# Kernel optimization log

Measured on AMD Instinct MI355X. Metric: run time of the kernel, lower is better.

The kernel has to match this reference:

```python
import jax, jax.numpy as jnp
import numpy as np

B, S, D = 4, 2048, 2048
E = 64           # num_experts
TOPK = 2         # num_experts_per_token


def setup_inputs() -> dict:
    key = jax.random.key(0)
    k1, k2, k3 = jax.random.split(key, 3)
    x_real = jax.random.normal(k1, (B, S, D), dtype=jnp.float32)
    x_imag = jax.random.normal(k2, (B, S, D), dtype=jnp.float32)
    # flax Dense: kernel [in_features, out_features] with lecun_normal-ish scale
    W = jax.random.normal(k3, (2 * D, E), dtype=jnp.float32) / np.sqrt(2.0 * D)
    b = jnp.zeros((E,), dtype=jnp.float32)
    return {"x_real": x_real, "x_imag": x_imag, "W": W, "b": b}


def reference(x_real, x_imag, W, b):
    # amp = |x|, phase = angle(x) for x = x_real + i*x_imag
    amp = jnp.hypot(x_real, x_imag)                 # [B,S,D]
    phase = jnp.arctan2(x_imag, x_real)             # [B,S,D]
    routing_input = jnp.concatenate([amp, phase], axis=-1)  # [B,S,2D]
    scores = jnp.einsum('bsf,fe->bse', routing_input, W) + b  # [B,S,E]
    probs = jax.nn.softmax(scores, axis=-1)
    top_k_probs, top_k_indices = jax.lax.top_k(probs, TOPK)   # [B,S,K]
    top_k_probs = top_k_probs / jnp.sum(top_k_probs, axis=-1, keepdims=True)
    return (top_k_probs, top_k_indices)
```

## Files before the change

kernel.cpp:

```cpp
#include <hip/hip_runtime.h>
#include <math.h>

#define NTOK 8192
#define DD   2048
#define EE   64
#define TSTRIP 16
#define NCH 16
#define PROB_N (NTOK*2)
#define AROW 136
#define F_PSTRIDE (128*4*64*8)

typedef _Float16 f16x8 __attribute__((ext_vector_type(8)));
typedef _Float16 f16x4 __attribute__((ext_vector_type(4)));
typedef float    f32x4 __attribute__((ext_vector_type(4)));

__device__ __forceinline__ float fast_atan2f(float y, float x) {
    const float ax = __builtin_fabsf(x), ay = __builtin_fabsf(y);
    const float hi = fmaxf(ax, ay), lo = fminf(ax, ay);
    const bool  big = lo > 0.4142135679721832f * hi;
    const float num = big ? (lo - hi) : lo;
    const float den = big ? (lo + hi) : hi;
    float rc = __builtin_amdgcn_rcpf(den);
    rc = rc * fmaf(-den, rc, 2.0f);
    const float z  = num * rc;
    const float z2 = z * z;
    float p = fmaf(z2, 8.05374449538e-2f, -1.38776856032e-1f);
    p = fmaf(z2, p, 1.99777106478e-1f);
    p = fmaf(z2, p, -3.33329491539e-1f);
    float r = fmaf(z * z2, p, z);
    r = r + (big ? 0.78539816339744830962f : 0.0f);
    r = (ay > ax) ? (1.57079632679489661923f - r) : r;
    r = (x < 0.0f) ? (3.14159265358979323846f - r) : r;
    return copysignf(r, y);
}

__device__ __forceinline__ void fsplit2(float x, _Float16& h1, _Float16& h2s) {
    const _Float16 a = (_Float16)x;
    h1 = a;
    h2s = (_Float16)((x - (float)a) * 2048.0f);
}

__global__ __launch_bounds__(256) void wsplit(const float* __restrict__ W,
                                              _Float16* __restrict__ F) {
    const int g  = blockIdx.x * 256 + threadIdx.x;
    const int e  = g & 63;
    const int q  = g >> 6;
    const int d0 = q * 4;
    const int nt = e >> 4;
    const int lane = ((d0 & 31) >> 3) * 16 + (e & 15);
    const int j0 = d0 & 7;
    const int cka = 2 * (d0 >> 5);

    f16x4 a1, a2, p1, p2;
    #pragma unroll
    for (int i = 0; i < 4; ++i) {
        _Float16 h, l;
        fsplit2(W[(size_t)(d0 + i) * EE + e], h, l);      a1[i] = h; a2[i] = l;
        fsplit2(W[(size_t)(DD + d0 + i) * EE + e], h, l); p1[i] = h; p2[i] = l;
    }
    *(f16x4*)&F[((size_t)(0 * 128 + cka)     * 4 + nt) * 512 + lane * 8 + j0] = a1;
    *(f16x4*)&F[((size_t)(1 * 128 + cka)     * 4 + nt) * 512 + lane * 8 + j0] = a2;
    *(f16x4*)&F[((size_t)(0 * 128 + cka + 1) * 4 + nt) * 512 + lane * 8 + j0] = p1;
    *(f16x4*)&F[((size_t)(1 * 128 + cka + 1) * 4 + nt) * 512 + lane * 8 + j0] = p2;
}

__global__ __launch_bounds__(512, 4) void gemm_topk(
    const float* __restrict__ xr, const float* __restrict__ xi,
    const _Float16* __restrict__ F, const float* __restrict__ bias,
    float* __restrict__ out)
{
    __shared__ __align__(16) _Float16 A[2][2][2][TSTRIP][AROW];
    __shared__ float scoreH[2][TSTRIP][EE];

    const int tid = threadIdx.x;
    const int t0  = blockIdx.x * TSTRIP;
    const int wv = tid >> 6, lane = tid & 63;
    const int nt = wv & 3, kh = wv >> 2;
    const int fm = lane & 15, fq = lane >> 4;
    const int kh_s  = tid >> 8;
    const int tok_s = (tid >> 4) & 15;
    const int f4    = tid & 15;

    const float bv = bias[lane];

    const float* prx = xr + (size_t)(t0 + tok_s) * DD + kh_s * 1024 + f4 * 4;
    const float* pix = xi + (size_t)(t0 + tok_s) * DD + kh_s * 1024 + f4 * 4;
    const int posa = 64 * (f4 >> 3) + (f4 & 7) * 4;

    auto sprocess = [&](float4 vr, float4 vi, int buf) {
        const float ar[4] = {vr.x, vr.y, vr.z, vr.w};
        const float ai[4] = {vi.x, vi.y, vi.z, vi.w};
        f16x4 a1, a2, p1, p2;
        #pragma unroll
        for (int i = 0; i < 4; ++i) {
            const float amp = __builtin_amdgcn_sqrtf(fmaf(ar[i], ar[i], ai[i] * ai[i]));
            const float ph  = fast_atan2f(ai[i], ar[i]);
            _Float16 h, l;
            fsplit2(amp, h, l); a1[i] = h; a2[i] = l;
            fsplit2(ph,  h, l); p1[i] = h; p2[i] = l;
        }
        *(f16x4*)&A[buf][kh_s][0][tok_s][posa]      = a1;
        *(f16x4*)&A[buf][kh_s][1][tok_s][posa]      = a2;
        *(f16x4*)&A[buf][kh_s][0][tok_s][posa + 32] = p1;
        *(f16x4*)&A[buf][kh_s][1][tok_s][posa + 32] = p2;
    };

    f32x4 accH = (f32x4){0.f, 0.f, 0.f, 0.f};
    f32x4 accL = (f32x4){0.f, 0.f, 0.f, 0.f};

    sprocess(*(const float4*)prx, *(const float4*)pix, 0);
    __syncthreads();

    for (int c = 0; c < NCH; ++c) {
        const int buf = c & 1;
        float4 nvr, nvi;
        if (c + 1 < NCH) {
            nvr = *(const float4*)(prx + (c + 1) * 64);
            nvi = *(const float4*)(pix + (c + 1) * 64);
        }
        const int ck0 = kh * 64 + c * 4;
        const _Float16* b1p = F + ((size_t)ck0 * 4 + nt) * 512 + lane * 8;
        const _Float16* b2p = b1p + F_PSTRIDE;
        f16x8 b1[4], b2[4], a1[4], a2[4];
        #pragma unroll
        for (int j = 0; j < 4; ++j) {
            b1[j] = *(const f16x8*)(b1p + j * 2048);
            b2[j] = *(const f16x8*)(b2p + j * 2048);
        }
        #pragma unroll
        for (int j = 0; j < 4; ++j) {
            a1[j] = *(const f16x8*)&A[buf][kh][0][fm][j * 32 + fq * 8];
            a2[j] = *(const f16x8*)&A[buf][kh][1][fm][j * 32 + fq * 8];
        }
        #pragma unroll
        for (int j = 0; j < 4; ++j) {
            accH = __builtin_amdgcn_mfma_f32_16x16x32_f16(a1[j], b1[j], accH, 0, 0, 0);
            accL = __builtin_amdgcn_mfma_f32_16x16x32_f16(a1[j], b2[j], accL, 0, 0, 0);
            accL = __builtin_amdgcn_mfma_f32_16x16x32_f16(a2[j], b1[j], accL, 0, 0, 0);
        }
        if (c + 1 < NCH) sprocess(nvr, nvi, buf ^ 1);
        __syncthreads();
    }

    #pragma unroll
    for (int r = 0; r < 4; ++r)
        scoreH[kh][fq * 4 + r][nt * 16 + fm] = fmaf(accL[r], 4.8828125e-4f, accH[r]);
    __syncthreads();

    #pragma unroll
    for (int rep = 0; rep < 2; ++rep) {
        const int tok = wv * 2 + rep;
        float v1 = scoreH[0][tok][lane] + scoreH[1][tok][lane] + bv;
        float v2 = -INFINITY;
        int   i1 = lane, i2 = 64;
        #pragma unroll
        for (int off = 1; off < 64; off <<= 1) {
            const float ov1 = __shfl_xor(v1, off, 64);
            const int   oi1 = __shfl_xor(i1, off, 64);
            const float ov2 = __shfl_xor(v2, off, 64);
            const int   oi2 = __shfl_xor(i2, off, 64);
            const bool b1 = (ov1 > v1) || (ov1 == v1 && oi1 < i1);
            const float n1 = b1 ? ov1 : v1;  const int ni1 = b1 ? oi1 : i1;
            const float c1 = b1 ? v1  : ov1; const int ci1 = b1 ? i1  : oi1;
            const float c2 = b1 ? ov2 : v2;  const int ci2 = b1 ? oi2 : i2;
            const bool b2 = (c1 > c2) || (c1 == c2 && ci1 < ci2);
            v1 = n1; i1 = ni1;
            v2 = b2 ? c1 : c2; i2 = b2 ? ci1 : ci2;
        }
        if (lane == 0) {
            const int t = t0 + tok;
            const float z  = expf(v2 - v1);
            const float p1 = 1.0f / (1.0f + z);
            const float p2 = z / (1.0f + z);
            out[(size_t)t * 2 + 0] = p1;
            out[(size_t)t * 2 + 1] = p2;
            out[PROB_N + (size_t)t * 2 + 0] = (float)i1;
            out[PROB_N + (size_t)t * 2 + 1] = (float)i2;
        }
    }
}

extern "C" void kernel_launch(void* const* d_in, const int* in_sizes, int n_in,
                              void* d_out, int out_size, void* d_ws, size_t ws_size,
                              hipStream_t stream) {
    const float* xr = (const float*)d_in[0];
    const float* xi = (const float*)d_in[1];
    const float* W  = (const float*)d_in[2];
    const float* b  = (const float*)d_in[3];
    float* out = (float*)d_out;
    _Float16* F = (_Float16*)d_ws;

    wsplit<<<128, 256, 0, stream>>>(W, F);
    gemm_topk<<<NTOK / TSTRIP, 512, 0, stream>>>(xr, xi, F, b, out);
}
```

Before: 173.7 us.

## Register double-buffer weight fragments and use lightweight LDS-only barriers

Prefetches the next chunk's weight fragments from global memory into a second register buffer while the current chunk's MFMAs run, so the matrix ops no longer wait on global loads issued in the same iteration. The main loop is fully unrolled, and __syncthreads is replaced by waiting only on LDS counters plus s_barrier, so outstanding global loads are not drained at each barrier. This raises register pressure (two sets of B fragments), which could affect occupancy under launch_bounds(512,4).

```diff
diff --git a/kernel.cpp b/kernel.cpp
--- a/kernel.cpp
+++ b/kernel.cpp
@@ -108,38 +108,54 @@
     f32x4 accH = (f32x4){0.f, 0.f, 0.f, 0.f};
     f32x4 accL = (f32x4){0.f, 0.f, 0.f, 0.f};
 
-    sprocess(*(const float4*)prx, *(const float4*)pix, 0);
-    __syncthreads();
-
+    const _Float16* bbase = F + ((size_t)(kh * 64) * 4 + nt) * 512 + lane * 8;
+
+    f16x8 bh[2][4], bl[2][4];
+
+    {
+        const float4 vr0 = *(const float4*)prx;
+        const float4 vi0 = *(const float4*)pix;
+        #pragma unroll
+        for (int j = 0; j < 4; ++j) {
+            bh[0][j] = *(const f16x8*)(bbase + j * 2048);
+            bl[0][j] = *(const f16x8*)(bbase + F_PSTRIDE + j * 2048);
+        }
+        sprocess(vr0, vi0, 0);
+    }
+    asm volatile("s_waitcnt lgkmcnt(0)" ::: "memory");
+    __builtin_amdgcn_s_barrier();
+    asm volatile("" ::: "memory");
+
+    #pragma unroll
     for (int c = 0; c < NCH; ++c) {
-        const int buf = c & 1;
+        const int buf  = c & 1;
+        const int nbuf = buf ^ 1;
+        const bool more = (c + 1 < NCH);
         float4 nvr, nvi;
-        if (c + 1 < NCH) {
+        if (more) {
             nvr = *(const float4*)(prx + (c + 1) * 64);
             nvi = *(const float4*)(pix + (c + 1) * 64);
-        }
-        const int ck0 = kh * 64 + c * 4;
-        const _Float16* b1p = F + ((size_t)ck0 * 4 + nt) * 512 + lane * 8;
-        const _Float16* b2p = b1p + F_PSTRIDE;
-        f16x8 b1[4], b2[4], a1[4], a2[4];
+            const _Float16* nb = bbase + (size_t)(c + 1) * 8192;
+            #pragma unroll
+            for (int j = 0; j < 4; ++j) {
+                bh[nbuf][j] = *(const f16x8*)(nb + j * 2048);
+                bl[nbuf][j] = *(const f16x8*)(nb + F_PSTRIDE + j * 2048);
+            }
+        }
         #pragma unroll
         for (int j = 0; j < 4; ++j) {
-            b1[j] = *(const f16x8*)(b1p + j * 2048);
-            b2[j] = *(const f16x8*)(b2p + j * 2048);
-        }
-        #pragma unroll
-        for (int j = 0; j < 4; ++j) {
-            a1[j] = *(const f16x8*)&A[buf][kh][0][fm][j * 32 + fq * 8];
-            a2[j] = *(const f16x8*)&A[buf][kh][1][fm][j * 32 + fq * 8];
-        }
-        #pragma unroll
-        for (int j = 0; j < 4; ++j) {
-            accH = __builtin_amdgcn_mfma_f32_16x16x32_f16(a1[j], b1[j], accH, 0, 0, 0);
-            accL = __builtin_amdgcn_mfma_f32_16x16x32_f16(a1[j], b2[j], accL, 0, 0, 0);
-            accL = __builtin_amdgcn_mfma_f32_16x16x32_f16(a2[j], b1[j], accL, 0, 0, 0);
-        }
-        if (c + 1 < NCH) sprocess(nvr, nvi, buf ^ 1);
-        __syncthreads();
+            const f16x8 a1 = *(const f16x8*)&A[buf][kh][0][fm][j * 32 + fq * 8];
+            const f16x8 a2 = *(const f16x8*)&A[buf][kh][1][fm][j * 32 + fq * 8];
+            accH = __builtin_amdgcn_mfma_f32_16x16x32_f16(a1, bh[buf][j], accH, 0, 0, 0);
+            accL = __builtin_amdgcn_mfma_f32_16x16x32_f16(a1, bl[buf][j], accL, 0, 0, 0);
+            accL = __builtin_amdgcn_mfma_f32_16x16x32_f16(a2, bh[buf][j], accL, 0, 0, 0);
+        }
+        if (more) {
+            sprocess(nvr, nvi, nbuf);
+            asm volatile("s_waitcnt lgkmcnt(0)" ::: "memory");
+            __builtin_amdgcn_s_barrier();
+            asm volatile("" ::: "memory");
+        }
     }
 
     #pragma unroll
```

New measurement: 164.1 us. -5.5%, faster.

## Load activations directly into MFMA registers and split K across all eight waves

Applied to the files above, without the earlier changes.

Each wave now reads its own slice of x straight from global memory in the MFMA A-fragment layout, computes amp/phase and the fp16 split in registers, and multiplies against all four expert tiles. This removes the shared-memory staging buffer and the per-chunk __syncthreads. Partial scores from the eight K-slices are reduced through shared memory before top-k. In exchange, each wave loads all four B tiles, which adds global traffic per wave, and it holds more accumulators, which raises register pressure. The occupancy hint in launch_bounds is also dropped.

```diff
diff --git a/kernel.cpp b/kernel.cpp
--- a/kernel.cpp
+++ b/kernel.cpp
@@ -5,9 +5,7 @@
 #define DD   2048
 #define EE   64
 #define TSTRIP 16
-#define NCH 16
 #define PROB_N (NTOK*2)
-#define AROW 136
 #define F_PSTRIDE (128*4*64*8)
 
 typedef _Float16 f16x8 __attribute__((ext_vector_type(8)));
@@ -64,93 +62,85 @@
     *(f16x4*)&F[((size_t)(1 * 128 + cka + 1) * 4 + nt) * 512 + lane * 8 + j0] = p2;
 }
 
-__global__ __launch_bounds__(512, 4) void gemm_topk(
+__global__ __launch_bounds__(512) void gemm_topk(
     const float* __restrict__ xr, const float* __restrict__ xi,
     const _Float16* __restrict__ F, const float* __restrict__ bias,
     float* __restrict__ out)
 {
-    __shared__ __align__(16) _Float16 A[2][2][2][TSTRIP][AROW];
-    __shared__ float scoreH[2][TSTRIP][EE];
+    __shared__ float scoreP[8][TSTRIP][EE];
 
     const int tid = threadIdx.x;
     const int t0  = blockIdx.x * TSTRIP;
     const int wv = tid >> 6, lane = tid & 63;
-    const int nt = wv & 3, kh = wv >> 2;
     const int fm = lane & 15, fq = lane >> 4;
-    const int kh_s  = tid >> 8;
-    const int tok_s = (tid >> 4) & 15;
-    const int f4    = tid & 15;
 
-    const float bv = bias[lane];
+    const float* prx = xr + (size_t)(t0 + fm) * DD + wv * 256 + fq * 8;
+    const float* pix = xi + (size_t)(t0 + fm) * DD + wv * 256 + fq * 8;
 
-    const float* prx = xr + (size_t)(t0 + tok_s) * DD + kh_s * 1024 + f4 * 4;
-    const float* pix = xi + (size_t)(t0 + tok_s) * DD + kh_s * 1024 + f4 * 4;
-    const int posa = 64 * (f4 >> 3) + (f4 & 7) * 4;
+    f32x4 accH[4], accL[4];
+    #pragma unroll
+    for (int nt = 0; nt < 4; ++nt) {
+        accH[nt] = (f32x4){0.f, 0.f, 0.f, 0.f};
+        accL[nt] = (f32x4){0.f, 0.f, 0.f, 0.f};
+    }
 
-    auto sprocess = [&](float4 vr, float4 vi, int buf) {
-        const float ar[4] = {vr.x, vr.y, vr.z, vr.w};
-        const float ai[4] = {vi.x, vi.y, vi.z, vi.w};
-        f16x4 a1, a2, p1, p2;
+    #pragma unroll 2
+    for (int p = 0; p < 8; ++p) {
+        const float4 r0 = *(const float4*)(prx + p * 32);
+        const float4 r1 = *(const float4*)(prx + p * 32 + 4);
+        const float4 i0 = *(const float4*)(pix + p * 32);
+        const float4 i1 = *(const float4*)(pix + p * 32 + 4);
+
+        f16x8 a1, a2, q1, q2;
         #pragma unroll
-        for (int i = 0; i < 4; ++i) {
-            const float amp = __builtin_amdgcn_sqrtf(fmaf(ar[i], ar[i], ai[i] * ai[i]));
-            const float ph  = fast_atan2f(ai[i], ar[i]);
-            _Float16 h, l;
-            fsplit2(amp, h, l); a1[i] = h; a2[i] = l;
-            fsplit2(ph,  h, l); p1[i] = h; p2[i] = l;
+        for (int h = 0; h < 2; ++h) {
+            const float4 vr = h ? r1 : r0;
+            const float4 vi = h ? i1 : i0;
+            const float ar[4] = {vr.x, vr.y, vr.z, vr.w};
+            const float ai[4] = {vi.x, vi.y, vi.z, vi.w};
+            #pragma unroll
+            for (int i = 0; i < 4; ++i) {
+                const float amp = __builtin_amdgcn_sqrtf(fmaf(ar[i], ar[i], ai[i] * ai[i]));
+                const float ph  = fast_atan2f(ai[i], ar[i]);
+                _Float16 hh, ll;
+                fsplit2(amp, hh, ll); a1[h * 4 + i] = hh; a2[h * 4 + i] = ll;
+                fsplit2(ph,  hh, ll); q1[h * 4 + i] = hh; q2[h * 4 + i] = ll;
+            }
         }
-        *(f16x4*)&A[buf][kh_s][0][tok_s][posa]      = a1;
-        *(f16x4*)&A[buf][kh_s][1][tok_s][posa]      = a2;
-        *(f16x4*)&A[buf][kh_s][0][tok_s][posa + 32] = p1;
-        *(f16x4*)&A[buf][kh_s][1][tok_s][posa + 32] = p2;
-    };
 
-    f32x4 accH = (f32x4){0.f, 0.f, 0.f, 0.f};
-    f32x4 accL = (f32x4){0.f, 0.f, 0.f, 0.f};
-
-    sprocess(*(const float4*)prx, *(const float4*)pix, 0);
-    __syncthreads();
-
-    for (int c = 0; c < NCH; ++c) {
-        const int buf = c & 1;
-        float4 nvr, nvi;
-        if (c + 1 < NCH) {
-            nvr = *(const float4*)(prx + (c + 1) * 64);
-            nvi = *(const float4*)(pix + (c + 1) * 64);
+        const int ck = (wv * 8 + p) * 2;
+        const _Float16* bp = F + ((size_t)ck * 4) * 512 + lane * 8;
+        #pragma unroll
+        for (int nt = 0; nt < 4; ++nt) {
+            const _Float16* qp = bp + nt * 512;
+            const f16x8 b1a = *(const f16x8*)(qp);
+            const f16x8 b2a = *(const f16x8*)(qp + F_PSTRIDE);
+            const f16x8 b1p = *(const f16x8*)(qp + 2048);
+            const f16x8 b2p = *(const f16x8*)(qp + 2048 + F_PSTRIDE);
+            accH[nt] = __builtin_amdgcn_mfma_f32_16x16x32_f16(a1, b1a, accH[nt], 0, 0, 0);
+            accL[nt] = __builtin_amdgcn_mfma_f32_16x16x32_f16(a1, b2a, accL[nt], 0, 0, 0);
+            accL[nt] = __builtin_amdgcn_mfma_f32_16x16x32_f16(a2, b1a, accL[nt], 0, 0, 0);
+            accH[nt] = __builtin_amdgcn_mfma_f32_16x16x32_f16(q1, b1p, accH[nt], 0, 0, 0);
+            accL[nt] = __builtin_amdgcn_mfma_f32_16x16x32_f16(q1, b2p, accL[nt], 0, 0, 0);
+            accL[nt] = __builtin_amdgcn_mfma_f32_16x16x32_f16(q2, b1p, accL[nt], 0, 0, 0);
         }
-        const int ck0 = kh * 64 + c * 4;
-        const _Float16* b1p = F + ((size_t)ck0 * 4 + nt) * 512 + lane * 8;
-        const _Float16* b2p = b1p + F_PSTRIDE;
-        f16x8 b1[4], b2[4], a1[4], a2[4];
-        #pragma unroll
-        for (int j = 0; j < 4; ++j) {
-            b1[j] = *(const f16x8*)(b1p + j * 2048);
-            b2[j] = *(const f16x8*)(b2p + j * 2048);
-        }
-        #pragma unroll
-        for (int j = 0; j < 4; ++j) {
-            a1[j] = *(const f16x8*)&A[buf][kh][0][fm][j * 32 + fq * 8];
-            a2[j] = *(const f16x8*)&A[buf][kh][1][fm][j * 32 + fq * 8];
-        }
-        #pragma unroll
-        for (int j = 0; j < 4; ++j) {
-            accH = __builtin_amdgcn_mfma_f32_16x16x32_f16(a1[j], b1[j], accH, 0, 0, 0);
-            accL = __builtin_amdgcn_mfma_f32_16x16x32_f16(a1[j], b2[j], accL, 0, 0, 0);
-            accL = __builtin_amdgcn_mfma_f32_16x16x32_f16(a2[j], b1[j], accL, 0, 0, 0);
-        }
-        if (c + 1 < NCH) sprocess(nvr, nvi, buf ^ 1);
-        __syncthreads();
     }
 
     #pragma unroll
-    for (int r = 0; r < 4; ++r)
-        scoreH[kh][fq * 4 + r][nt * 16 + fm] = fmaf(accL[r], 4.8828125e-4f, accH[r]);
+    for (int nt = 0; nt < 4; ++nt)
+        #pragma unroll
+        for (int r = 0; r < 4; ++r)
+            scoreP[wv][fq * 4 + r][nt * 16 + fm] =
+                fmaf(accL[nt][r], 4.8828125e-4f, accH[nt][r]);
     __syncthreads();
 
+    const float bv = bias[lane];
     #pragma unroll
     for (int rep = 0; rep < 2; ++rep) {
         const int tok = wv * 2 + rep;
-        float v1 = scoreH[0][tok][lane] + scoreH[1][tok][lane] + bv;
+        float v1 = bv;
+        #pragma unroll
+        for (int kq = 0; kq < 8; ++kq) v1 += scoreP[kq][tok][lane];
         float v2 = -INFINITY;
         int   i1 = lane, i2 = 64;
         #pragma unroll
```

After: 175.2 us. No clear change (+0.9%).
